# Kernel optimization log

Measured on AMD Instinct MI355X. Metric: run time of the kernel, lower is better.

The kernel has to match this reference:

```python
import jax, jax.numpy as jnp
import numpy as np

B, Z, LIN = 256, 512, 4096
N_SLOTS = 256          # next_pow_2: padded tree slots (slot 0 = zero vector)
L = 3 * (N_SLOTS - 1)  # 765 gather indices (3 per internal node)
CH = [16, 32, 64, 128, 256, 512, 512]  # conv channel chain, last = output_dim


def mish(x):
    return x * jnp.tanh(jax.nn.softplus(x))


def tree_layer_norm(x):
    # normalize each tree over (channels, nodes); torch.std is unbiased (ddof=1)
    mean = jnp.mean(x, axis=(1, 2), keepdims=True)
    std = jnp.std(x, axis=(1, 2), ddof=1, keepdims=True)
    return (x - mean) / (std + 1e-5)


def binary_tree_conv(x, idx, w, b):
    # x: [B, Cin, N]; idx: [B, L]; w: [Cout, Cin, 3]; b: [Cout]
    Bc, C, _ = x.shape
    g = jnp.take_along_axis(
        x, jnp.broadcast_to(idx[:, None, :], (Bc, C, idx.shape[1])), axis=2)
    g = g.reshape(Bc, C, -1, 3)                       # [B, Cin, N-1, 3]
    out = jnp.einsum('bcnk,ock->bon', g, w) + b[None, :, None]
    zero = jnp.zeros((Bc, w.shape[0], 1), out.dtype)  # re-attach zero slot
    return jnp.concatenate([zero, out], axis=2)       # [B, Cout, N]


def setup_inputs() -> dict:
    key = jax.random.key(0)
    ks = jax.random.split(key, 32)
    inp = {}
    inp['trees'] = jax.random.normal(ks[0], (B, Z), jnp.float32)
    idx = jax.random.randint(ks[1], (B, L, 1), 0, N_SLOTS, dtype=jnp.int64 if jax.config.jax_enable_x64 else jnp.int32)
    idx = idx.at[0, 0, 0].set(N_SLOTS - 1)  # guarantee next_pow_2 == 256
    inp['indexes'] = idx
    inp['W_lin'] = jax.random.normal(ks[2], (LIN, Z), jnp.float32) / np.float32(np.sqrt(Z))
    inp['b_lin'] = jax.random.normal(ks[3], (LIN,), jnp.float32) * 0.01
    inp['bn_gamma'] = jax.random.uniform(ks[4], (LIN,), jnp.float32, 0.5, 1.5)
    inp['bn_beta'] = jax.random.normal(ks[5], (LIN,), jnp.float32) * 0.1
    inp['bn_mean'] = jax.random.normal(ks[6], (LIN,), jnp.float32) * 0.1
    inp['bn_var'] = jax.random.uniform(ks[7], (LIN,), jnp.float32, 0.5, 1.5)
    for i in range(6):
        cin, cout = CH[i], CH[i + 1]
        inp[f'w{i}'] = jax.random.normal(ks[8 + 2 * i], (cout, cin, 3), jnp.float32) / np.float32(np.sqrt(3 * cin))
        inp[f'bc{i}'] = jax.random.normal(ks[9 + 2 * i], (cout,), jnp.float32) * 0.01
    return inp


def reference(trees, indexes, W_lin, b_lin, bn_gamma, bn_beta, bn_mean, bn_var,
              w0, bc0, w1, bc1, w2, bc2, w3, bc3, w4, bc4, w5, bc5):
    next_pow_2 = 1 << int(np.asarray(jnp.max(indexes)).item()).bit_length()
    # linear -> BatchNorm1d (eval, running stats) -> Mish -> Dropout(eval = identity)
    x = trees @ W_lin.T + b_lin
    x = (x - bn_mean) * jax.lax.rsqrt(bn_var + 1e-5) * bn_gamma + bn_beta
    x = mish(x)
    x = x.reshape(x.shape[0], LIN // next_pow_2, next_pow_2)  # [B, 16, 256]
    idx = indexes[:, :, 0]
    layers = [(w0, bc0, False), (w1, bc1, True), (w2, bc2, True),
              (w3, bc3, True), (w4, bc4, True), (w5, bc5, True)]
    for w, b, act in layers:
        x = tree_layer_norm(binary_tree_conv(x, idx, w, b))
        if act:
            x = mish(x)
    return x  # [B, output_dim, 256] (the tensor part of the (data, indexes) tuple)
```

## Files before the change

### kernel.cpp

```cpp
#include <hip/hip_runtime.h>
#include <hip/hip_bf16.h>

typedef __attribute__((ext_vector_type(8))) short bf16x8;
typedef __attribute__((ext_vector_type(4))) float f32x4;

__device__ __forceinline__ float b2f(unsigned int u) {
  union { unsigned int i; float f; } v; v.i = u << 16; return v.f;
}
__device__ __forceinline__ unsigned short f2b(float f) {
  unsigned int x = __float_as_uint(f);
  unsigned int r = (x + 0x7fffu + ((x >> 16) & 1u)) >> 16;
  return (unsigned short)r;
}
__device__ __forceinline__ float mish_f(float x) {
  float sp = (x > 20.f) ? x : log1pf(expf(x));
  return x * tanhf(sp);
}

__global__ __launch_bounds__(256) void detect_flags(
    const unsigned short* __restrict__ trees_u16,
    const unsigned int* __restrict__ idx_u32, int* __restrict__ flags)
{
  __shared__ int cnt_sane, cnt_nz;
  const int tid = threadIdx.x;
  if (tid == 0) { cnt_sane = 0; cnt_nz = 0; }
  __syncthreads();
  int sane = 0;
  for (int i = tid; i < 2048; i += 256) {
    unsigned short w = trees_u16[i];
    unsigned int e = (w >> 7) & 0xFFu;
    if ((w & 0x7FFFu) == 0 || (e >= 117u && e <= 133u)) sane++;
  }
  atomicAdd(&cnt_sane, sane);
  int nz = 0;
  for (int i = tid; i < 4096; i += 256) {
    if (idx_u32[2 * i + 1] != 0u) nz++;
  }
  atomicAdd(&cnt_nz, nz);
  __syncthreads();
  if (tid == 0) {
    flags[0] = (cnt_sane < 1843) ? 1 : 0;
    flags[1] = (cnt_nz == 0) ? 1 : 0;
  }
}

__global__ __launch_bounds__(256) void linear_bn_mish(
    const void* __restrict__ treesv, const void* __restrict__ Wlv,
    const void* __restrict__ blv, const void* __restrict__ gamv,
    const void* __restrict__ betv, const void* __restrict__ muv,
    const void* __restrict__ varv, unsigned short* __restrict__ out,
    const int* __restrict__ flags)
{
  __shared__ float As[16][64];
  __shared__ float Bs[16][64];
  const int F = flags[0];
  const int tid = threadIdx.x;
  const int tx = tid & 15, ty = tid >> 4;
  const int j0 = blockIdx.x * 64, b0 = blockIdx.y * 64;
  const int lr = tid >> 2, lc = (tid & 3) << 2;
  const unsigned short* t16 = (const unsigned short*)treesv;
  const float* t32 = (const float*)treesv;
  const unsigned short* w16 = (const unsigned short*)Wlv;
  const float* w32 = (const float*)Wlv;
  float acc[4][4] = {};
  for (int k0 = 0; k0 < 512; k0 += 16) {
    float a0, a1, a2, a3, q0, q1, q2, q3;
    if (F) {
      float4 ta = *(const float4*)(t32 + (b0 + lr) * 512 + k0 + lc);
      float4 tb = *(const float4*)(w32 + (j0 + lr) * 512 + k0 + lc);
      a0 = ta.x; a1 = ta.y; a2 = ta.z; a3 = ta.w;
      q0 = tb.x; q1 = tb.y; q2 = tb.z; q3 = tb.w;
    } else {
      ushort4 ta = *(const ushort4*)(t16 + (b0 + lr) * 512 + k0 + lc);
      ushort4 tb = *(const ushort4*)(w16 + (j0 + lr) * 512 + k0 + lc);
      a0 = b2f(ta.x); a1 = b2f(ta.y); a2 = b2f(ta.z); a3 = b2f(ta.w);
      q0 = b2f(tb.x); q1 = b2f(tb.y); q2 = b2f(tb.z); q3 = b2f(tb.w);
    }
    __syncthreads();
    As[lc + 0][lr] = a0; As[lc + 1][lr] = a1; As[lc + 2][lr] = a2; As[lc + 3][lr] = a3;
    Bs[lc + 0][lr] = q0; Bs[lc + 1][lr] = q1; Bs[lc + 2][lr] = q2; Bs[lc + 3][lr] = q3;
    __syncthreads();
#pragma unroll
    for (int kk = 0; kk < 16; ++kk) {
      float4 av = *(const float4*)&As[kk][ty * 4];
      float4 bv = *(const float4*)&Bs[kk][tx * 4];
      float a[4] = {av.x, av.y, av.z, av.w};
      float bb[4] = {bv.x, bv.y, bv.z, bv.w};
#pragma unroll
      for (int iy = 0; iy < 4; ++iy)
#pragma unroll
        for (int jx = 0; jx < 4; ++jx) acc[iy][jx] += a[iy] * bb[jx];
    }
  }
  const unsigned short* bl16 = (const unsigned short*)blv;  const float* bl32 = (const float*)blv;
  const unsigned short* g16 = (const unsigned short*)gamv;  const float* g32 = (const float*)gamv;
  const unsigned short* be16 = (const unsigned short*)betv; const float* be32 = (const float*)betv;
  const unsigned short* m16 = (const unsigned short*)muv;   const float* m32 = (const float*)muv;
  const unsigned short* v16 = (const unsigned short*)varv;  const float* v32 = (const float*)varv;
#pragma unroll
  for (int iy = 0; iy < 4; ++iy) {
    int b = b0 + ty * 4 + iy;
    unsigned short st[4];
#pragma unroll
    for (int jx = 0; jx < 4; ++jx) {
      int j = j0 + tx * 4 + jx;
      float bj = F ? bl32[j] : b2f(bl16[j]);
      float gj = F ? g32[j] : b2f(g16[j]);
      float ej = F ? be32[j] : b2f(be16[j]);
      float mj = F ? m32[j] : b2f(m16[j]);
      float vj = F ? v32[j] : b2f(v16[j]);
      float v = acc[iy][jx] + bj;
      v = (v - mj) * rsqrtf(vj + 1e-5f) * gj + ej;
      v = mish_f(v);
      st[jx] = f2b(v);
    }
    ushort4 pack; pack.x = st[0]; pack.y = st[1]; pack.z = st[2]; pack.w = st[3];
    *(ushort4*)(out + b * 4096 + j0 + tx * 4) = pack;
  }
}

template<int CIN, int COUT, int TO>
__global__ __launch_bounds__(256) void tree_conv(
    const unsigned short* __restrict__ xin,
    const void* __restrict__ idxv,
    const void* __restrict__ wv,
    const void* __restrict__ biasv,
    unsigned short* __restrict__ out,
    const int* __restrict__ flags)
{
  constexpr int CC = 16;
  constexpr int KC = CC * 3;
  constexpr int UO = TO / 16;
  constexpr int PE = (TO * KC) / 256;
  __shared__ float xs[CC][256];
  __shared__ float wsm[KC][TO];
  const int F = flags[0], G = flags[1];
  const int tid = threadIdx.x;
  const int tx = tid & 15, ty = tid >> 4;
  const int b = blockIdx.z;
  const int o0 = blockIdx.y * TO;
  const int n0 = blockIdx.x * 64;
  const unsigned short* xb = xin + b * CIN * 256;
  const unsigned short* wt16 = (const unsigned short*)wv;
  const float* wt32 = (const float*)wv;
  const int* idx32 = (const int*)idxv;

  int jj[4][3];
  int np[4];
  {
    const int step = G ? 2 : 1;
    const int* idxb = idx32 + b * 765 * step;
#pragma unroll
    for (int ni = 0; ni < 4; ++ni) {
      int n = n0 + tx * 4 + ni;
      np[ni] = n;
      int m = n - 1;
#pragma unroll
      for (int k = 0; k < 3; ++k) jj[ni][k] = (m >= 0) ? idxb[(3 * m + k) * step] : 0;
    }
  }

  float acc[UO][4];
#pragma unroll
  for (int u = 0; u < UO; ++u)
#pragma unroll
    for (int ni = 0; ni < 4; ++ni) acc[u][ni] = 0.f;

  for (int c0 = 0; c0 < CIN; c0 += CC) {
    __syncthreads();
    {
      const uint4* src = (const uint4*)(xb + c0 * 256);
      uint4 v0 = src[tid * 2];
      uint4 v1 = src[tid * 2 + 1];
      unsigned int ww[8] = {v0.x, v0.y, v0.z, v0.w, v1.x, v1.y, v1.z, v1.w};
      float t[16];
#pragma unroll
      for (int q = 0; q < 8; ++q) {
        t[2 * q] = b2f(ww[q] & 0xffffu);
        t[2 * q + 1] = b2f(ww[q] >> 16);
      }
      float* dst = &xs[tid >> 4][(tid & 15) * 16];
#pragma unroll
      for (int q = 0; q < 4; ++q)
        *(float4*)(dst + 4 * q) = make_float4(t[4 * q], t[4 * q + 1], t[4 * q + 2], t[4 * q + 3]);
    }
    if (F) {
#pragma unroll
      for (int e = 0; e < PE; ++e) {
        int p = e * 256 + tid;
        int o_rel = p / KC;
        int rem = p - o_rel * KC;
        wsm[rem][o_rel] = wt32[(o0 + o_rel) * CIN * 3 + c0 * 3 + rem];
      }
    } else {
#pragma unroll
      for (int e = 0; e < PE; ++e) {
        int p = e * 256 + tid;
        int o_rel = p / KC;
        int rem = p - o_rel * KC;
        wsm[rem][o_rel] = b2f(wt16[(o0 + o_rel) * CIN * 3 + c0 * 3 + rem]);
      }
    }
    __syncthreads();
#pragma unroll
    for (int cc = 0; cc < CC; ++cc) {
      float wvv[3][UO];
#pragma unroll
      for (int k = 0; k < 3; ++k) {
        if constexpr (UO == 4) {
          float4 f = *(const float4*)&wsm[cc * 3 + k][ty * 4];
          wvv[k][0] = f.x; wvv[k][1] = f.y; wvv[k][2] = f.z; wvv[k][3] = f.w;
        } else {
          float2 f = *(const float2*)&wsm[cc * 3 + k][ty * 2];
          wvv[k][0] = f.x; wvv[k][1] = f.y;
        }
      }
#pragma unroll
      for (int ni = 0; ni < 4; ++ni) {
        float x0 = xs[cc][jj[ni][0]];
        float x1 = xs[cc][jj[ni][1]];
        float x2 = xs[cc][jj[ni][2]];
#pragma unroll
        for (int u = 0; u < UO; ++u)
          acc[u][ni] += wvv[0][u] * x0 + wvv[1][u] * x1 + wvv[2][u] * x2;
      }
    }
  }
  const unsigned short* bi16 = (const unsigned short*)biasv;
  const float* bi32 = (const float*)biasv;
#pragma unroll
  for (int u = 0; u < UO; ++u) {
    int o = o0 + ty * UO + u;
    float bv = F ? bi32[o] : b2f(bi16[o]);
    unsigned short st[4];
#pragma unroll
    for (int ni = 0; ni < 4; ++ni) {
      float v = (np[ni] == 0) ? 0.f : (acc[u][ni] + bv);
      st[ni] = f2b(v);
    }
    ushort4 pack; pack.x = st[0]; pack.y = st[1]; pack.z = st[2]; pack.w = st[3];
    *(ushort4*)(out + (b * COUT + o) * 256 + n0 + tx * 4) = pack;
  }
}

__global__ __launch_bounds__(256) void wt_transpose(
    const void* __restrict__ wv, unsigned short* __restrict__ Wt,
    int CIN, int COUT, const int* __restrict__ flags)
{
  const int K = CIN * 3;
  const int total = COUT * K;
  int gid = blockIdx.x * 256 + threadIdx.x;
  if (gid >= total) return;
  const int F = flags[0];
  int o = gid / K;
  int kp = gid - o * K;
  int cc0 = kp / 96;
  int rem = kp - cc0 * 96;
  int k = rem >> 5, ci = rem & 31;
  int c = cc0 * 32 + ci;
  int src = (o * CIN + c) * 3 + k;
  unsigned short v = F ? f2b(((const float*)wv)[src]) : ((const unsigned short*)wv)[src];
  Wt[gid] = v;
}

template<int CIN, int COUT>
__global__ __launch_bounds__(256) void tree_conv_mfma(
    const unsigned short* __restrict__ xT,
    const void* __restrict__ idxv,
    const unsigned short* __restrict__ Wt,
    const void* __restrict__ biasv,
    unsigned short* __restrict__ outT,
    const int* __restrict__ flags)
{
  constexpr int K = CIN * 3;
  constexpr int XS = 40;
  constexpr int WS = 104;
  __shared__ unsigned short xTl[256 * XS];
  __shared__ unsigned short Wl[128 * WS];
  const int tid = threadIdx.x;
  const int wave = tid >> 6, lane = tid & 63, quad = lane >> 4, l15 = lane & 15;

  const int BPB = gridDim.x * gridDim.y;
  const unsigned raw = blockIdx.x + gridDim.x * (blockIdx.y + gridDim.y * blockIdx.z);
  const int r8 = (int)(raw & 7u);
  const unsigned m9 = raw >> 3;
  const int b = r8 * 32 + (int)(m9 / (unsigned)BPB);
  const int u = (int)(m9 % (unsigned)BPB);
  const int n_blk = (u & 1) * 128, o_blk = (u >> 1) * 128;

  const int o_half = (wave >> 1) * 64, n_half = (wave & 1) * 64;
  const int F = flags[0], G = flags[1];

  int jr[4][3];
  int ng[4];
  {
    const int step = G ? 2 : 1;
    const int* idxb = (const int*)idxv + (size_t)b * 765 * step;
#pragma unroll
    for (int t = 0; t < 4; ++t) {
      int n = n_blk + n_half + t * 16 + l15;
      ng[t] = n;
      int mm = n - 1;
#pragma unroll
      for (int k = 0; k < 3; ++k) jr[t][k] = (mm >= 0) ? idxb[(3 * mm + k) * step] : 0;
    }
  }

  f32x4 acc[4][4];
#pragma unroll
  for (int a = 0; a < 4; ++a)
#pragma unroll
    for (int c = 0; c < 4; ++c) acc[a][c] = (f32x4){0.f, 0.f, 0.f, 0.f};

  const unsigned short* xsrc = xT + ((size_t)b * 256 + tid) * CIN;
  const int wo = tid >> 1, wpart = tid & 1;
  const unsigned short* wsrc = Wt + (size_t)(o_blk + wo) * K + wpart * 48;

  uint4 xr0, xr1, xr2, xr3, wr0, wr1, wr2, wr3, wr4, wr5;
  {
    const unsigned short* s = xsrc;
    xr0 = *(const uint4*)(s);      xr1 = *(const uint4*)(s + 8);
    xr2 = *(const uint4*)(s + 16); xr3 = *(const uint4*)(s + 24);
    const unsigned short* w = wsrc;
    wr0 = *(const uint4*)(w);      wr1 = *(const uint4*)(w + 8);
    wr2 = *(const uint4*)(w + 16); wr3 = *(const uint4*)(w + 24);
    wr4 = *(const uint4*)(w + 32); wr5 = *(const uint4*)(w + 40);
  }

  for (int c0 = 0; c0 < CIN; c0 += 32) {
    __syncthreads();
    *(uint4*)&xTl[tid * XS + 0]  = xr0;
    *(uint4*)&xTl[tid * XS + 8]  = xr1;
    *(uint4*)&xTl[tid * XS + 16] = xr2;
    *(uint4*)&xTl[tid * XS + 24] = xr3;
    {
      unsigned short* d = &Wl[wo * WS + wpart * 48];
      *(uint4*)(d + 0)  = wr0;
      *(uint4*)(d + 8)  = wr1;
      *(uint4*)(d + 16) = wr2;
      *(uint4*)(d + 24) = wr3;
      *(uint4*)(d + 32) = wr4;
      *(uint4*)(d + 40) = wr5;
    }
    __syncthreads();
    if (c0 + 32 < CIN) {
      const unsigned short* s = xsrc + c0 + 32;
      xr0 = *(const uint4*)(s);      xr1 = *(const uint4*)(s + 8);
      xr2 = *(const uint4*)(s + 16); xr3 = *(const uint4*)(s + 24);
      const unsigned short* w = wsrc + (size_t)(c0 + 32) * 3;
      wr0 = *(const uint4*)(w);      wr1 = *(const uint4*)(w + 8);
      wr2 = *(const uint4*)(w + 16); wr3 = *(const uint4*)(w + 24);
      wr4 = *(const uint4*)(w + 32); wr5 = *(const uint4*)(w + 40);
    }
#pragma unroll
    for (int k = 0; k < 3; ++k) {
      bf16x8 af[4], bfr[4];
#pragma unroll
      for (int t = 0; t < 4; ++t)
        af[t] = *(const bf16x8*)&Wl[(o_half + t * 16 + l15) * WS + k * 32 + quad * 8];
#pragma unroll
      for (int t = 0; t < 4; ++t)
        bfr[t] = *(const bf16x8*)&xTl[jr[t][k] * XS + quad * 8];
#pragma unroll
      for (int to = 0; to < 4; ++to)
#pragma unroll
        for (int tn = 0; tn < 4; ++tn)
          acc[to][tn] = __builtin_amdgcn_mfma_f32_16x16x32_bf16(
              af[to], bfr[tn], acc[to][tn], 0, 0, 0);
    }
  }

  const unsigned short* bi16 = (const unsigned short*)biasv;
  const float* bi32 = (const float*)biasv;
#pragma unroll
  for (int to = 0; to < 4; ++to) {
    int og = o_blk + o_half + to * 16 + quad * 4;
    float b4[4];
#pragma unroll
    for (int r = 0; r < 4; ++r) b4[r] = F ? bi32[og + r] : b2f(bi16[og + r]);
#pragma unroll
    for (int tn = 0; tn < 4; ++tn) {
      int n = ng[tn];
      ushort4 st;
      if (n == 0) {
        st.x = 0; st.y = 0; st.z = 0; st.w = 0;
      } else {
        st.x = f2b(acc[to][tn][0] + b4[0]);
        st.y = f2b(acc[to][tn][1] + b4[1]);
        st.z = f2b(acc[to][tn][2] + b4[2]);
        st.w = f2b(acc[to][tn][3] + b4[3]);
      }
      *(ushort4*)(outT + ((size_t)b * 256 + n) * COUT + og) = st;
    }
  }
}

__global__ __launch_bounds__(256) void stats_part(
    const unsigned short* __restrict__ raw, int C, float* __restrict__ partials)
{
  const int tid = threadIdx.x;
  const int sidx = blockIdx.x, b = blockIdx.y;
  const int NS = gridDim.x;
  const int nv = C * 32;
  const int per = nv / NS;
  const uint4* pv = (const uint4*)(raw + (size_t)b * C * 256) + (size_t)sidx * per;
  float s = 0.f, s2 = 0.f;
  for (int i = tid; i < per; i += 256) {
    uint4 v = pv[i];
    unsigned int ww[4] = {v.x, v.y, v.z, v.w};
#pragma unroll
    for (int q = 0; q < 4; ++q) {
      float f0 = b2f(ww[q] & 0xffffu), f1 = b2f(ww[q] >> 16);
      s += f0 + f1; s2 += f0 * f0 + f1 * f1;
    }
  }
  __shared__ float rs[256], rs2[256];
  rs[tid] = s; rs2[tid] = s2;
  __syncthreads();
  for (int off = 128; off > 0; off >>= 1) {
    if (tid < off) { rs[tid] += rs[tid + off]; rs2[tid] += rs2[tid + off]; }
    __syncthreads();
  }
  if (tid == 0) {
    partials[2 * (b * NS + sidx) + 0] = rs[0];
    partials[2 * (b * NS + sidx) + 1] = rs2[0];
  }
}

__global__ __launch_bounds__(256) void stats_fin(
    const float* __restrict__ partials, int C, int NS, float* __restrict__ stats)
{
  const int b = threadIdx.x;
  float s = 0.f, s2 = 0.f;
  for (int i = 0; i < NS; ++i) {
    s += partials[2 * (b * NS + i) + 0];
    s2 += partials[2 * (b * NS + i) + 1];
  }
  const float M = (float)(C * 256);
  float mean = s / M;
  float varv = (s2 - s * s / M) / (M - 1.f);
  varv = fmaxf(varv, 0.f);
  stats[2 * b] = mean;
  stats[2 * b + 1] = 1.f / (sqrtf(varv) + 1e-5f);
}

__global__ __launch_bounds__(256) void apply_norm(
    const unsigned short* __restrict__ raw, unsigned short* __restrict__ out,
    int C, int act, const float* __restrict__ stats)
{
  const int tid = threadIdx.x;
  const int b = blockIdx.y;
  const int nv = C * 32;
  const float mean = stats[2 * b], inv = stats[2 * b + 1];
  const uint4* pv = (const uint4*)(raw + (size_t)b * C * 256);
  uint4* ov = (uint4*)(out + (size_t)b * C * 256);
  const int stride = gridDim.x * 256;
  for (int i = blockIdx.x * 256 + tid; i < nv; i += stride) {
    uint4 v = pv[i];
    unsigned int ww[4] = {v.x, v.y, v.z, v.w};
    unsigned int rr[4];
#pragma unroll
    for (int q = 0; q < 4; ++q) {
      float f0 = (b2f(ww[q] & 0xffffu) - mean) * inv;
      float f1 = (b2f(ww[q] >> 16) - mean) * inv;
      if (act) { f0 = mish_f(f0); f1 = mish_f(f1); }
      rr[q] = (unsigned)f2b(f0) | ((unsigned)f2b(f1) << 16);
    }
    uint4 r; r.x = rr[0]; r.y = rr[1]; r.z = rr[2]; r.w = rr[3];
    ov[i] = r;
  }
}

__global__ __launch_bounds__(256) void apply_t(
    const unsigned short* __restrict__ in, void* __restrict__ outv,
    int R, int S, int act, int finalw,
    const float* __restrict__ stats, const int* __restrict__ flags)
{
  __shared__ unsigned short tile[64 * 72];
  const int tid = threadIdx.x;
  const int b = blockIdx.z;
  const int S0 = blockIdx.x * 64, R0 = blockIdx.y * 64;
  const float mean = stats[2 * b], inv = stats[2 * b + 1];
  {
    int r = tid >> 2, c4 = (tid & 3) * 16;
    const unsigned short* src = in + ((size_t)b * R + R0 + r) * S + S0 + c4;
    uint4 u0 = *(const uint4*)src;
    uint4 u1 = *(const uint4*)(src + 8);
    unsigned int ww[8] = {u0.x, u0.y, u0.z, u0.w, u1.x, u1.y, u1.z, u1.w};
    unsigned short tv[16];
#pragma unroll
    for (int q = 0; q < 8; ++q) {
      float f0 = (b2f(ww[q] & 0xffffu) - mean) * inv;
      float f1 = (b2f(ww[q] >> 16) - mean) * inv;
      if (act) { f0 = mish_f(f0); f1 = mish_f(f1); }
      tv[2 * q] = f2b(f0);
      tv[2 * q + 1] = f2b(f1);
    }
    unsigned short* d = &tile[r * 72 + c4];
#pragma unroll
    for (int q = 0; q < 2; ++q) {
      ushort4 p0; p0.x = tv[8*q+0]; p0.y = tv[8*q+1]; p0.z = tv[8*q+2]; p0.w = tv[8*q+3];
      ushort4 p1; p1.x = tv[8*q+4]; p1.y = tv[8*q+5]; p1.z = tv[8*q+6]; p1.w = tv[8*q+7];
      *(ushort4*)(d + 8 * q) = p0;
      *(ushort4*)(d + 8 * q + 4) = p1;
    }
  }
  __syncthreads();
  {
    int s = tid >> 2, rc = (tid & 3) * 16;
    const int wf32 = finalw && flags[0];
    if (wf32) {
      float* of = (float*)outv + ((size_t)b * S + S0 + s) * R + R0 + rc;
#pragma unroll
      for (int q = 0; q < 4; ++q) {
        float4 fv;
        fv.x = b2f(tile[(rc + 4 * q + 0) * 72 + s]);
        fv.y = b2f(tile[(rc + 4 * q + 1) * 72 + s]);
        fv.z = b2f(tile[(rc + 4 * q + 2) * 72 + s]);
        fv.w = b2f(tile[(rc + 4 * q + 3) * 72 + s]);
        *(float4*)(of + 4 * q) = fv;
      }
    } else {
      unsigned short* ob = (unsigned short*)outv + ((size_t)b * S + S0 + s) * R + R0 + rc;
#pragma unroll
      for (int q = 0; q < 4; ++q) {
        ushort4 p;
        p.x = tile[(rc + 4 * q + 0) * 72 + s];
        p.y = tile[(rc + 4 * q + 1) * 72 + s];
        p.z = tile[(rc + 4 * q + 2) * 72 + s];
        p.w = tile[(rc + 4 * q + 3) * 72 + s];
        *(ushort4*)(ob + 4 * q) = p;
      }
    }
  }
}

extern "C" void kernel_launch(void* const* d_in, const int* in_sizes, int n_in,
                              void* d_out, int out_size, void* d_ws, size_t ws_size,
                              hipStream_t stream) {
  const void* trees = d_in[0];
  const void* indexes = d_in[1];
  const void* W_lin = d_in[2];
  const void* b_lin = d_in[3];
  const void* gam = d_in[4];
  const void* bet = d_in[5];
  const void* mu  = d_in[6];
  const void* var = d_in[7];
  const void* w0 = d_in[8];   const void* bc0 = d_in[9];
  const void* w1 = d_in[10];  const void* bc1 = d_in[11];
  const void* w2 = d_in[12];  const void* bc2 = d_in[13];
  const void* w3 = d_in[14];  const void* bc3 = d_in[15];
  const void* w4 = d_in[16];  const void* bc4 = d_in[17];
  const void* w5 = d_in[18];  const void* bc5 = d_in[19];

  int* flags = (int*)d_ws;
  unsigned short* nrm = (unsigned short*)((char*)d_ws + 1024);
  unsigned short* raw = nrm + 33554432;
  float* statsF = (float*)((char*)d_ws + 1024 + 67108864 - 2048);
  unsigned short* Wt = (unsigned short*)d_out;
  float* partials = (float*)((char*)d_out + (4 << 20));
  float* stats2 = (float*)((char*)d_out + (4 << 20) + 65536);

  detect_flags<<<1, 256, 0, stream>>>((const unsigned short*)trees,
                                      (const unsigned int*)indexes, flags);

  linear_bn_mish<<<dim3(64, 4), 256, 0, stream>>>(trees, W_lin, b_lin, gam, bet, mu, var,
                                                  nrm, flags);

  tree_conv<16, 32, 32><<<dim3(4, 1, 256), 256, 0, stream>>>(nrm, indexes, w0, bc0, raw, flags);
  stats_part<<<dim3(4, 256), 256, 0, stream>>>(raw, 32, partials);
  stats_fin<<<1, 256, 0, stream>>>(partials, 32, 4, stats2);
  apply_norm<<<dim3(4, 256), 256, 0, stream>>>(raw, nrm, 32, 0, stats2);

  tree_conv<32, 64, 64><<<dim3(4, 1, 256), 256, 0, stream>>>(nrm, indexes, w1, bc1, raw, flags);
  stats_part<<<dim3(8, 256), 256, 0, stream>>>(raw, 64, partials);
  stats_fin<<<1, 256, 0, stream>>>(partials, 64, 8, stats2);
  apply_t<<<dim3(4, 1, 256), 256, 0, stream>>>(raw, nrm, 64, 256, 1, 0, stats2, flags);

  wt_transpose<<<96, 256, 0, stream>>>(w2, Wt, 64, 128, flags);
  tree_conv_mfma<64, 128><<<dim3(2, 1, 256), 256, 0, stream>>>(nrm, indexes, Wt, bc2, raw, flags);
  stats_part<<<dim3(8, 256), 256, 0, stream>>>(raw, 128, partials);
  stats_fin<<<1, 256, 0, stream>>>(partials, 128, 8, stats2);
  apply_norm<<<dim3(8, 256), 256, 0, stream>>>(raw, nrm, 128, 1, stats2);

  wt_transpose<<<384, 256, 0, stream>>>(w3, Wt, 128, 256, flags);
  tree_conv_mfma<128, 256><<<dim3(2, 2, 256), 256, 0, stream>>>(nrm, indexes, Wt, bc3, raw, flags);
  stats_part<<<dim3(16, 256), 256, 0, stream>>>(raw, 256, partials);
  stats_fin<<<1, 256, 0, stream>>>(partials, 256, 16, stats2);
  apply_norm<<<dim3(8, 256), 256, 0, stream>>>(raw, nrm, 256, 1, stats2);

  wt_transpose<<<1536, 256, 0, stream>>>(w4, Wt, 256, 512, flags);
  tree_conv_mfma<256, 512><<<dim3(2, 4, 256), 256, 0, stream>>>(nrm, indexes, Wt, bc4, raw, flags);
  stats_part<<<dim3(16, 256), 256, 0, stream>>>(raw, 512, partials);
  stats_fin<<<1, 256, 0, stream>>>(partials, 512, 16, stats2);
  apply_norm<<<dim3(16, 256), 256, 0, stream>>>(raw, nrm, 512, 1, stats2);

  wt_transpose<<<3072, 256, 0, stream>>>(w5, Wt, 512, 512, flags);
  tree_conv_mfma<512, 512><<<dim3(2, 4, 256), 256, 0, stream>>>(nrm, indexes, Wt, bc5, raw, flags);
  stats_part<<<dim3(16, 256), 256, 0, stream>>>(raw, 512, partials);
  stats_fin<<<1, 256, 0, stream>>>(partials, 512, 16, statsF);
  apply_t<<<dim3(8, 4, 256), 256, 0, stream>>>(raw, d_out, 256, 512, 1, 1, statsF, flags);
}
```

Baseline: 983.5 us.

## Widen MFMA tree-conv blocks to 512 threads covering all 256 nodes

Each tree-conv MFMA block now runs 8 waves and covers all 256 node slots for a 128-output-channel tile, instead of 4 waves covering half the nodes. The two node halves therefore share one staged copy of the weight tile in LDS, halving weight global loads and removing the duplicate x-staging done by sibling blocks. Per-thread staging loads shrink to match the larger block. The cost is a larger block with more barrier participants, launch bounds of (512, 4) that cap registers, and half as many blocks in the grid.

```diff
diff --git a/kernel.cpp b/kernel.cpp
--- a/kernel.cpp
+++ b/kernel.cpp
@@ -264,7 +264,7 @@
 }
 
 template<int CIN, int COUT>
-__global__ __launch_bounds__(256) void tree_conv_mfma(
+__global__ __launch_bounds__(512, 4) void tree_conv_mfma(
     const unsigned short* __restrict__ xT,
     const void* __restrict__ idxv,
     const unsigned short* __restrict__ Wt,
@@ -280,15 +280,16 @@
   const int tid = threadIdx.x;
   const int wave = tid >> 6, lane = tid & 63, quad = lane >> 4, l15 = lane & 15;
 
-  const int BPB = gridDim.x * gridDim.y;
-  const unsigned raw = blockIdx.x + gridDim.x * (blockIdx.y + gridDim.y * blockIdx.z);
+  const int BPB = gridDim.y;
+  const unsigned raw = blockIdx.y + gridDim.y * blockIdx.z;
   const int r8 = (int)(raw & 7u);
   const unsigned m9 = raw >> 3;
   const int b = r8 * 32 + (int)(m9 / (unsigned)BPB);
   const int u = (int)(m9 % (unsigned)BPB);
-  const int n_blk = (u & 1) * 128, o_blk = (u >> 1) * 128;
-
-  const int o_half = (wave >> 1) * 64, n_half = (wave & 1) * 64;
+  const int o_blk = u * 128;
+
+  const int o_half = (wave >> 2) * 64;
+  const int n_sub = (wave & 3) * 64;
   const int F = flags[0], G = flags[1];
 
   int jr[4][3];
@@ -298,7 +299,7 @@
     const int* idxb = (const int*)idxv + (size_t)b * 765 * step;
 #pragma unroll
     for (int t = 0; t < 4; ++t) {
-      int n = n_blk + n_half + t * 16 + l15;
+      int n = n_sub + t * 16 + l15;
       ng[t] = n;
       int mm = n - 1;
 #pragma unroll
@@ -312,45 +313,39 @@
 #pragma unroll
     for (int c = 0; c < 4; ++c) acc[a][c] = (f32x4){0.f, 0.f, 0.f, 0.f};
 
-  const unsigned short* xsrc = xT + ((size_t)b * 256 + tid) * CIN;
-  const int wo = tid >> 1, wpart = tid & 1;
-  const unsigned short* wsrc = Wt + (size_t)(o_blk + wo) * K + wpart * 48;
-
-  uint4 xr0, xr1, xr2, xr3, wr0, wr1, wr2, wr3, wr4, wr5;
+  const int xrow = tid >> 1, xcol = (tid & 1) * 16;
+  const unsigned short* xsrc = xT + ((size_t)b * 256 + xrow) * CIN + xcol;
+  const int wo = tid >> 2, wq = tid & 3;
+  const unsigned short* wsrc = Wt + (size_t)(o_blk + wo) * K + wq * 24;
+
+  uint4 xr0, xr1, wr0, wr1, wr2;
   {
-    const unsigned short* s = xsrc;
-    xr0 = *(const uint4*)(s);      xr1 = *(const uint4*)(s + 8);
-    xr2 = *(const uint4*)(s + 16); xr3 = *(const uint4*)(s + 24);
-    const unsigned short* w = wsrc;
-    wr0 = *(const uint4*)(w);      wr1 = *(const uint4*)(w + 8);
-    wr2 = *(const uint4*)(w + 16); wr3 = *(const uint4*)(w + 24);
-    wr4 = *(const uint4*)(w + 32); wr5 = *(const uint4*)(w + 40);
+    xr0 = *(const uint4*)(xsrc);
+    xr1 = *(const uint4*)(xsrc + 8);
+    wr0 = *(const uint4*)(wsrc);
+    wr1 = *(const uint4*)(wsrc + 8);
+    wr2 = *(const uint4*)(wsrc + 16);
   }
 
   for (int c0 = 0; c0 < CIN; c0 += 32) {
     __syncthreads();
-    *(uint4*)&xTl[tid * XS + 0]  = xr0;
-    *(uint4*)&xTl[tid * XS + 8]  = xr1;
-    *(uint4*)&xTl[tid * XS + 16] = xr2;
-    *(uint4*)&xTl[tid * XS + 24] = xr3;
+    *(uint4*)&xTl[xrow * XS + xcol + 0] = xr0;
+    *(uint4*)&xTl[xrow * XS + xcol + 8] = xr1;
     {
-      unsigned short* d = &Wl[wo * WS + wpart * 48];
+      unsigned short* d = &Wl[wo * WS + wq * 24];
       *(uint4*)(d + 0)  = wr0;
       *(uint4*)(d + 8)  = wr1;
       *(uint4*)(d + 16) = wr2;
-      *(uint4*)(d + 24) = wr3;
-      *(uint4*)(d + 32) = wr4;
-      *(uint4*)(d + 40) = wr5;
     }
     __syncthreads();
     if (c0 + 32 < CIN) {
       const unsigned short* s = xsrc + c0 + 32;
-      xr0 = *(const uint4*)(s);      xr1 = *(const uint4*)(s + 8);
-      xr2 = *(const uint4*)(s + 16); xr3 = *(const uint4*)(s + 24);
+      xr0 = *(const uint4*)(s);
+      xr1 = *(const uint4*)(s + 8);
       const unsigned short* w = wsrc + (size_t)(c0 + 32) * 3;
-      wr0 = *(const uint4*)(w);      wr1 = *(const uint4*)(w + 8);
-      wr2 = *(const uint4*)(w + 16); wr3 = *(const uint4*)(w + 24);
-      wr4 = *(const uint4*)(w + 32); wr5 = *(const uint4*)(w + 40);
+      wr0 = *(const uint4*)(w);
+      wr1 = *(const uint4*)(w + 8);
+      wr2 = *(const uint4*)(w + 16);
     }
 #pragma unroll
     for (int k = 0; k < 3; ++k) {
@@ -578,25 +573,25 @@
   apply_t<<<dim3(4, 1, 256), 256, 0, stream>>>(raw, nrm, 64, 256, 1, 0, stats2, flags);
 
   wt_transpose<<<96, 256, 0, stream>>>(w2, Wt, 64, 128, flags);
-  tree_conv_mfma<64, 128><<<dim3(2, 1, 256), 256, 0, stream>>>(nrm, indexes, Wt, bc2, raw, flags);
+  tree_conv_mfma<64, 128><<<dim3(1, 1, 256), 512, 0, stream>>>(nrm, indexes, Wt, bc2, raw, flags);
   stats_part<<<dim3(8, 256), 256, 0, stream>>>(raw, 128, partials);
   stats_fin<<<1, 256, 0, stream>>>(partials, 128, 8, stats2);
   apply_norm<<<dim3(8, 256), 256, 0, stream>>>(raw, nrm, 128, 1, stats2);
 
   wt_transpose<<<384, 256, 0, stream>>>(w3, Wt, 128, 256, flags);
-  tree_conv_mfma<128, 256><<<dim3(2, 2, 256), 256, 0, stream>>>(nrm, indexes, Wt, bc3, raw, flags);
+  tree_conv_mfma<128, 256><<<dim3(1, 2, 256), 512, 0, stream>>>(nrm, indexes, Wt, bc3, raw, flags);
   stats_part<<<dim3(16, 256), 256, 0, stream>>>(raw, 256, partials);
   stats_fin<<<1, 256, 0, stream>>>(partials, 256, 16, stats2);
   apply_norm<<<dim3(8, 256), 256, 0, stream>>>(raw, nrm, 256, 1, stats2);
 
   wt_transpose<<<1536, 256, 0, stream>>>(w4, Wt, 256, 512, flags);
-  tree_conv_mfma<256, 512><<<dim3(2, 4, 256), 256, 0, stream>>>(nrm, indexes, Wt, bc4, raw, flags);
+  tree_conv_mfma<256, 512><<<dim3(1, 4, 256), 512, 0, stream>>>(nrm, indexes, Wt, bc4, raw, flags);
   stats_part<<<dim3(16, 256), 256, 0, stream>>>(raw, 512, partials);
   stats_fin<<<1, 256, 0, stream>>>(partials, 512, 16, stats2);
   apply_norm<<<dim3(16, 256), 256, 0, stream>>>(raw, nrm, 512, 1, stats2);
 
   wt_transpose<<<3072, 256, 0, stream>>>(w5, Wt, 512, 512, flags);
-  tree_conv_mfma<512, 512><<<dim3(2, 4, 256), 256, 0, stream>>>(nrm, indexes, Wt, bc5, raw, flags);
+  tree_conv_mfma<512, 512><<<dim3(1, 4, 256), 512, 0, stream>>>(nrm, indexes, Wt, bc5, raw, flags);
   stats_part<<<dim3(16, 256), 256, 0, stream>>>(raw, 512, partials);
   stats_fin<<<1, 256, 0, stream>>>(partials, 512, 16, statsF);
   apply_t<<<dim3(8, 4, 256), 256, 0, stream>>>(raw, d_out, 256, 512, 1, 1, statsF, flags);
```

Result: slower. 1.042 ms (+5.9%).

## Pre-tile weights into MFMA fragment layout and load A operands directly to registers

Applied to the files above, without the earlier changes.

The weight transpose kernel now writes weights in 16x32 fragment tiles ordered by (o16, channel chunk, k), so each lane can load its MFMA A-fragment straight from global memory. The shared-memory weight tile and its staging stores are removed, which frees LDS and cuts LDS traffic. Each wave now loads its own weight fragments from global/L2, so the four waves' overlapping loads are duplicated and register pressure rises (12 bf16x8 fragments held). The gather offsets are also precomputed with the stride folded in.

```diff
diff --git a/kernel.cpp b/kernel.cpp
--- a/kernel.cpp
+++ b/kernel.cpp
@@ -252,12 +252,12 @@
   int gid = blockIdx.x * 256 + threadIdx.x;
   if (gid >= total) return;
   const int F = flags[0];
-  int o = gid / K;
-  int kp = gid - o * K;
-  int cc0 = kp / 96;
-  int rem = kp - cc0 * 96;
-  int k = rem >> 5, ci = rem & 31;
-  int c = cc0 * 32 + ci;
+  const int nch = CIN >> 5;
+  int tile = gid >> 9, within = gid & 511;
+  int r = within >> 5, cc = within & 31;
+  int k = tile % 3; int tmp = tile / 3;
+  int ch = tmp % nch; int o16 = tmp / nch;
+  int o = o16 * 16 + r, c = ch * 32 + cc;
   int src = (o * CIN + c) * 3 + k;
   unsigned short v = F ? f2b(((const float*)wv)[src]) : ((const unsigned short*)wv)[src];
   Wt[gid] = v;
@@ -272,11 +272,9 @@
     unsigned short* __restrict__ outT,
     const int* __restrict__ flags)
 {
-  constexpr int K = CIN * 3;
+  constexpr int NCH = CIN / 32;
   constexpr int XS = 40;
-  constexpr int WS = 104;
   __shared__ unsigned short xTl[256 * XS];
-  __shared__ unsigned short Wl[128 * WS];
   const int tid = threadIdx.x;
   const int wave = tid >> 6, lane = tid & 63, quad = lane >> 4, l15 = lane & 15;
 
@@ -291,7 +289,7 @@
   const int o_half = (wave >> 1) * 64, n_half = (wave & 1) * 64;
   const int F = flags[0], G = flags[1];
 
-  int jr[4][3];
+  int jroff[4][3];
   int ng[4];
   {
     const int step = G ? 2 : 1;
@@ -302,7 +300,10 @@
       ng[t] = n;
       int mm = n - 1;
 #pragma unroll
-      for (int k = 0; k < 3; ++k) jr[t][k] = (mm >= 0) ? idxb[(3 * mm + k) * step] : 0;
+      for (int k = 0; k < 3; ++k) {
+        int j = (mm >= 0) ? idxb[(3 * mm + k) * step] : 0;
+        jroff[t][k] = j * XS + quad * 8;
+      }
     }
   }
 
@@ -313,18 +314,20 @@
     for (int c = 0; c < 4; ++c) acc[a][c] = (f32x4){0.f, 0.f, 0.f, 0.f};
 
   const unsigned short* xsrc = xT + ((size_t)b * 256 + tid) * CIN;
-  const int wo = tid >> 1, wpart = tid & 1;
-  const unsigned short* wsrc = Wt + (size_t)(o_blk + wo) * K + wpart * 48;
-
-  uint4 xr0, xr1, xr2, xr3, wr0, wr1, wr2, wr3, wr4, wr5;
+  const unsigned short* wfrag = Wt + (size_t)((o_blk + o_half) >> 4) * NCH * 3 * 512
+                                + l15 * 32 + quad * 8;
+
+  uint4 xr0, xr1, xr2, xr3;
+  bf16x8 af[4][3];
   {
     const unsigned short* s = xsrc;
     xr0 = *(const uint4*)(s);      xr1 = *(const uint4*)(s + 8);
     xr2 = *(const uint4*)(s + 16); xr3 = *(const uint4*)(s + 24);
-    const unsigned short* w = wsrc;
-    wr0 = *(const uint4*)(w);      wr1 = *(const uint4*)(w + 8);
-    wr2 = *(const uint4*)(w + 16); wr3 = *(const uint4*)(w + 24);
-    wr4 = *(const uint4*)(w + 32); wr5 = *(const uint4*)(w + 40);
+#pragma unroll
+    for (int t = 0; t < 4; ++t)
+#pragma unroll
+      for (int k = 0; k < 3; ++k)
+        af[t][k] = *(const bf16x8*)(wfrag + (size_t)(t * NCH * 3 + k) * 512);
   }
 
   for (int c0 = 0; c0 < CIN; c0 += 32) {
@@ -333,40 +336,32 @@
     *(uint4*)&xTl[tid * XS + 8]  = xr1;
     *(uint4*)&xTl[tid * XS + 16] = xr2;
     *(uint4*)&xTl[tid * XS + 24] = xr3;
-    {
-      unsigned short* d = &Wl[wo * WS + wpart * 48];
-      *(uint4*)(d + 0)  = wr0;
-      *(uint4*)(d + 8)  = wr1;
-      *(uint4*)(d + 16) = wr2;
-      *(uint4*)(d + 24) = wr3;
-      *(uint4*)(d + 32) = wr4;
-      *(uint4*)(d + 40) = wr5;
-    }
     __syncthreads();
     if (c0 + 32 < CIN) {
       const unsigned short* s = xsrc + c0 + 32;
       xr0 = *(const uint4*)(s);      xr1 = *(const uint4*)(s + 8);
       xr2 = *(const uint4*)(s + 16); xr3 = *(const uint4*)(s + 24);
-      const unsigned short* w = wsrc + (size_t)(c0 + 32) * 3;
-      wr0 = *(const uint4*)(w);      wr1 = *(const uint4*)(w + 8);
-      wr2 = *(const uint4*)(w + 16); wr3 = *(const uint4*)(w + 24);
-      wr4 = *(const uint4*)(w + 32); wr5 = *(const uint4*)(w + 40);
     }
 #pragma unroll
     for (int k = 0; k < 3; ++k) {
-      bf16x8 af[4], bfr[4];
+      bf16x8 bfr[4];
 #pragma unroll
       for (int t = 0; t < 4; ++t)
-        af[t] = *(const bf16x8*)&Wl[(o_half + t * 16 + l15) * WS + k * 32 + quad * 8];
-#pragma unroll
-      for (int t = 0; t < 4; ++t)
-        bfr[t] = *(const bf16x8*)&xTl[jr[t][k] * XS + quad * 8];
+        bfr[t] = *(const bf16x8*)&xTl[jroff[t][k]];
 #pragma unroll
       for (int to = 0; to < 4; ++to)
 #pragma unroll
         for (int tn = 0; tn < 4; ++tn)
           acc[to][tn] = __builtin_amdgcn_mfma_f32_16x16x32_bf16(
-              af[to], bfr[tn], acc[to][tn], 0, 0, 0);
+              af[to][k], bfr[tn], acc[to][tn], 0, 0, 0);
+    }
+    if (c0 + 32 < CIN) {
+      const unsigned short* wch = wfrag + (size_t)((c0 >> 5) + 1) * 3 * 512;
+#pragma unroll
+      for (int t = 0; t < 4; ++t)
+#pragma unroll
+        for (int k = 0; k < 3; ++k)
+          af[t][k] = *(const bf16x8*)(wch + (size_t)(t * NCH * 3 + k) * 512);
     }
   }
 
```

After: 1.031 ms. 4.8% more time.
